# Kernel optimization log

Measured on AMD Instinct MI355X. Metric: run time of the kernel, lower is better.

The kernel has to match this reference:

```python
import jax, jax.numpy as jnp
import numpy as np

HID = 2048
HEADS = 16
HEAD = HID // HEADS  # 128
INTER = 8192
EPS = 1e-5
THETA = 10000.0
B, S = 2, 2048


def _layernorm(x, scale, bias):
    mu = jnp.mean(x, axis=-1, keepdims=True)
    var = jnp.var(x, axis=-1, keepdims=True)
    return (x - mu) * jax.lax.rsqrt(var + EPS) * scale + bias


def _rope(x, cos, sin):
    # x: [b,s,h,d]; adjacent pairs form complex numbers (per apply_rotary_emb)
    xr = x.reshape(*x.shape[:-1], HEAD // 2, 2)
    x0, x1 = xr[..., 0], xr[..., 1]
    o0 = x0 * cos - x1 * sin
    o1 = x0 * sin + x1 * cos
    return jnp.stack((o0, o1), axis=-1).reshape(x.shape)


def setup_inputs() -> dict:
    key = jax.random.key(0)
    ks = jax.random.split(key, 6)
    sc = 0.02
    return {
        "hidden_states": jax.random.normal(ks[0], (B, S, HID), jnp.float32),
        "attention_mask": jnp.zeros((B, 1, 1, S), jnp.float32),
        "w_qkv": (jax.random.normal(ks[1], (HID, 3 * HID), jnp.float32) * sc),
        "b_qkv": jnp.zeros((3 * HID,), jnp.float32),
        "w_o": (jax.random.normal(ks[2], (HID, HID), jnp.float32) * sc),
        "b_o": jnp.zeros((HID,), jnp.float32),
        "ln1_scale": jnp.ones((HID,), jnp.float32),
        "ln1_bias": jnp.zeros((HID,), jnp.float32),
        "ln2_scale": jnp.ones((HID,), jnp.float32),
        "ln2_bias": jnp.zeros((HID,), jnp.float32),
        "w_in": (jax.random.normal(ks[3], (HID, INTER), jnp.float32) * sc),
        "b_in": jnp.zeros((INTER,), jnp.float32),
        "w_out": (jax.random.normal(ks[4], (INTER, HID), jnp.float32) * sc),
        "b_out": jnp.zeros((HID,), jnp.float32),
    }


def reference(hidden_states, attention_mask, w_qkv, b_qkv, w_o, b_o,
              ln1_scale, ln1_bias, ln2_scale, ln2_bias,
              w_in, b_in, w_out, b_out):
    b, s, d = hidden_states.shape
    # ---- attention branch ----
    x1 = _layernorm(hidden_states, ln1_scale, ln1_bias)
    qkv = x1 @ w_qkv + b_qkv
    q, k, v = jnp.split(qkv, 3, axis=-1)
    q = q.reshape(b, s, HEADS, HEAD)
    k = k.reshape(b, s, HEADS, HEAD)
    v = v.reshape(b, s, HEADS, HEAD)
    # rotary embedding (complex pairing of adjacent elements)
    inv_freq = 1.0 / (THETA ** (jnp.arange(0, HEAD, 2, dtype=jnp.float32) / HEAD))
    freqs = jnp.arange(s, dtype=jnp.float32)[:, None] * inv_freq[None, :]  # [s, HEAD/2]
    cos = jnp.cos(freqs)[None, :, None, :]
    sin = jnp.sin(freqs)[None, :, None, :]
    q = _rope(q, cos, sin)
    k = _rope(k, cos, sin)
    # NOTE: source multiplies by sqrt(head_size) (faithful to original code)
    factor = jnp.sqrt(jnp.float32(HEAD))
    attn = jnp.einsum('bqhd,bkhd->bhqk', q, k) * factor  # [b,h,s,s]
    causal = jnp.tril(jnp.ones((s, s), dtype=bool))
    bias = jnp.where(causal, 0.0, jnp.finfo(jnp.float32).min)
    attn = attn + bias[None, None, :, :] + attention_mask
    p = jax.nn.softmax(attn, axis=-1)
    ao = jnp.einsum('bhqk,bkhd->bqhd', p, v).reshape(b, s, d)
    attn_out = ao @ w_o + b_o
    # ---- mlp branch (parallel residual) ----
    x2 = _layernorm(hidden_states, ln2_scale, ln2_bias)
    mlp = jax.nn.gelu(x2 @ w_in + b_in, approximate=False) @ w_out + b_out
    return mlp + hidden_states + attn_out
```

## Files before the change

kernel.cpp:

```cpp
#include <hip/hip_runtime.h>
#include <math.h>

#define HID 2048
#define NH 16
#define HD 128
#define INTER 8192
#define BB 2
#define SS 2048
#define MT (BB*SS)

typedef __bf16 bf16x8 __attribute__((ext_vector_type(8)));
typedef float f32x4 __attribute__((ext_vector_type(4)));
typedef unsigned short u16x8 __attribute__((ext_vector_type(8)));

__device__ __forceinline__ float bf2f(unsigned short u) {
  unsigned v = ((unsigned)u) << 16;
  return __builtin_bit_cast(float, v);
}
__device__ __forceinline__ unsigned short f2bf(float x) {
  unsigned u = __builtin_bit_cast(unsigned, x);
  u += 0x7fffu + ((u >> 16) & 1u);
  return (unsigned short)(u >> 16);
}
__device__ __forceinline__ void gll16(const void* g, const void* lds) {
  __builtin_amdgcn_global_load_lds(
      (const __attribute__((address_space(1))) void*)g,
      (__attribute__((address_space(3))) void*)lds, 16, 0, 0);
}

__global__ __launch_bounds__(256) void ln2k(
    const float* __restrict__ X, const float* __restrict__ s1,
    const float* __restrict__ b1, const float* __restrict__ s2,
    const float* __restrict__ b2, unsigned short* __restrict__ X1h,
    unsigned short* __restrict__ X1l, unsigned short* __restrict__ X2) {
  const int row = blockIdx.x;
  const int tid = threadIdx.x;
  const float* x = X + (long)row * HID;
  float4 v0 = ((const float4*)x)[tid * 2];
  float4 v1 = ((const float4*)x)[tid * 2 + 1];
  float s = v0.x + v0.y + v0.z + v0.w + v1.x + v1.y + v1.z + v1.w;
  float q = v0.x * v0.x + v0.y * v0.y + v0.z * v0.z + v0.w * v0.w +
            v1.x * v1.x + v1.y * v1.y + v1.z * v1.z + v1.w * v1.w;
#pragma unroll
  for (int off = 1; off < 64; off <<= 1) {
    s += __shfl_xor(s, off);
    q += __shfl_xor(q, off);
  }
  __shared__ float rs[4], rq[4];
  const int wid = tid >> 6, lane = tid & 63;
  if (lane == 0) { rs[wid] = s; rq[wid] = q; }
  __syncthreads();
  s = rs[0] + rs[1] + rs[2] + rs[3];
  q = rq[0] + rq[1] + rq[2] + rq[3];
  const float mu = s * (1.f / HID);
  const float var = q * (1.f / HID) - mu * mu;
  const float rstd = rsqrtf(var + 1e-5f);
  float xv[8] = {v0.x, v0.y, v0.z, v0.w, v1.x, v1.y, v1.z, v1.w};
  u16x8 o1h, o1l, o2;
#pragma unroll
  for (int e = 0; e < 8; e++) {
    const int j = tid * 8 + e;
    const float xn = (xv[e] - mu) * rstd;
    const float x1v = xn * s1[j] + b1[j];
    const unsigned short h = f2bf(x1v);
    o1h[e] = h;
    o1l[e] = f2bf(x1v - bf2f(h));
    o2[e] = f2bf(xn * s2[j] + b2[j]);
  }
  *(u16x8*)(X1h + (long)row * HID + tid * 8) = o1h;
  *(u16x8*)(X1l + (long)row * HID + tid * 8) = o1l;
  *(u16x8*)(X2 + (long)row * HID + tid * 8) = o2;
}

__global__ __launch_bounds__(256) void wtrans(const float* __restrict__ W,
                                              unsigned short* __restrict__ WT,
                                              int K, int N, int ldn, int coff) {
  (void)N;
  __shared__ float t[32][33];
  const int n0 = blockIdx.x * 32, k0 = blockIdx.y * 32;
  const int tx = threadIdx.x, ty = threadIdx.y;
#pragma unroll
  for (int r = 0; r < 4; r++)
    t[ty + r * 8][tx] = W[(long)(k0 + ty + r * 8) * ldn + coff + n0 + tx];
  __syncthreads();
#pragma unroll
  for (int r = 0; r < 4; r++)
    WT[(long)(n0 + ty + r * 8) * K + k0 + tx] = f2bf(t[tx][ty + r * 8]);
}

__global__ __launch_bounds__(256) void wtrans_hl(
    const float* __restrict__ W, unsigned short* __restrict__ WTh,
    unsigned short* __restrict__ WTl, int K, int ldn) {
  __shared__ float t[32][33];
  const int n0 = blockIdx.x * 32, k0 = blockIdx.y * 32;
  const int tx = threadIdx.x, ty = threadIdx.y;
#pragma unroll
  for (int r = 0; r < 4; r++)
    t[ty + r * 8][tx] = W[(long)(k0 + ty + r * 8) * ldn + n0 + tx];
  __syncthreads();
#pragma unroll
  for (int r = 0; r < 4; r++) {
    const float v = t[tx][ty + r * 8];
    const unsigned short h = f2bf(v);
    const long o = (long)(n0 + ty + r * 8) * K + k0 + tx;
    WTh[o] = h;
    WTl[o] = f2bf(v - bf2f(h));
  }
}

__global__ void rope_tab(float2* __restrict__ rope) {
  const int s = blockIdx.x, i = threadIdx.x;
  const double ang = (double)s * pow(10000.0, -(double)i / 64.0);
  rope[s * 64 + i] = make_float2((float)cos(ang), (float)sin(ang));
}

__global__ __launch_bounds__(256) void gemmqk(
    const unsigned short* __restrict__ Ah_, const unsigned short* __restrict__ Al_,
    const unsigned short* __restrict__ Bh_, const unsigned short* __restrict__ Bl_,
    const float* __restrict__ bias, const float2* __restrict__ rope,
    unsigned short* __restrict__ QH, unsigned short* __restrict__ QL,
    unsigned short* __restrict__ KH, unsigned short* __restrict__ KL) {
  __shared__ unsigned short Ash[128 * 64], Asl[128 * 64];
  __shared__ unsigned short Bsh[128 * 64], Bsl[128 * 64];
  const int K = HID;
  const int tid = threadIdx.x;
  const int wid = tid >> 6, lane = tid & 63;
  const int l16 = lane & 15, lhi = lane >> 4;
  const int bn = blockIdx.x, bm = blockIdx.y;
  const int wr = wid >> 1, wc = wid & 1;
  const long rA0 = (long)bm * 128;
  const long rB0 = (long)bn * 128;

  f32x4 acc[4][4] = {};

  for (int kt = 0; kt < K; kt += 64) {
#pragma unroll
    for (int i = 0; i < 4; i++) {
      const int lin = i * 4096 + wid * 1024 + (lane << 4);
      const int row = lin >> 7;
      const int cs = ((lin >> 4) & 7) ^ (row & 7);
      const int dst = i * 4096 + wid * 1024;
      const long ga = (rA0 + row) * (long)K + kt + cs * 8;
      const long gb = (rB0 + row) * (long)K + kt + cs * 8;
      gll16(Ah_ + ga, (const char*)Ash + dst);
      gll16(Al_ + ga, (const char*)Asl + dst);
      gll16(Bh_ + gb, (const char*)Bsh + dst);
      gll16(Bl_ + gb, (const char*)Bsl + dst);
    }
    __syncthreads();
#pragma unroll
    for (int ks = 0; ks < 2; ks++) {
      bf16x8 avh[4], avl[4], bvh[4], bvl[4];
#pragma unroll
      for (int m = 0; m < 4; m++) {
        const int row = wr * 64 + m * 16 + l16;
        const int ch = (ks * 4 + lhi) ^ (row & 7);
        avh[m] = *(const bf16x8*)((const char*)Ash + row * 128 + ch * 16);
        avl[m] = *(const bf16x8*)((const char*)Asl + row * 128 + ch * 16);
      }
#pragma unroll
      for (int n = 0; n < 4; n++) {
        const int row = wc * 64 + n * 16 + l16;
        const int ch = (ks * 4 + lhi) ^ (row & 7);
        bvh[n] = *(const bf16x8*)((const char*)Bsh + row * 128 + ch * 16);
        bvl[n] = *(const bf16x8*)((const char*)Bsl + row * 128 + ch * 16);
      }
#pragma unroll
      for (int m = 0; m < 4; m++)
#pragma unroll
        for (int n = 0; n < 4; n++) {
          acc[m][n] = __builtin_amdgcn_mfma_f32_16x16x32_bf16(avh[m], bvl[n],
                                                              acc[m][n], 0, 0, 0);
          acc[m][n] = __builtin_amdgcn_mfma_f32_16x16x32_bf16(avl[m], bvh[n],
                                                              acc[m][n], 0, 0, 0);
          acc[m][n] = __builtin_amdgcn_mfma_f32_16x16x32_bf16(avh[m], bvh[n],
                                                              acc[m][n], 0, 0, 0);
        }
    }
    __syncthreads();
  }

  const int b_ = (int)(rA0 >> 11);
#pragma unroll
  for (int m = 0; m < 4; m++) {
#pragma unroll
    for (int n = 0; n < 4; n++) {
      const int col = (int)rB0 + wc * 64 + n * 16 + l16;
      const float bsv = bias[col];
      const int i = (col & 127) >> 1;
      const int hh = (col >> 7) & 15;
      const int d = col & 127;
#pragma unroll
      for (int r = 0; r < 4; r++) {
        const int row = (int)rA0 + wr * 64 + m * 16 + lhi * 4 + r;
        const int srow = row & 2047;
        const float v = acc[m][n][r] + bsv;
        const float p = __shfl_xor(v, 1);
        const float2 cs = rope[srow * 64 + i];
        const float o = ((lane & 1) == 0) ? (v * cs.x - p * cs.y)
                                          : (p * cs.y + v * cs.x);
        const unsigned short hi = f2bf(o);
        const unsigned short lo = f2bf(o - bf2f(hi));
        const long dst = ((long)(b_ * NH + hh) * SS + srow) * HD + d;
        if (col < 2048) { QH[dst] = hi; QL[dst] = lo; }
        else            { KH[dst] = hi; KL[dst] = lo; }
      }
    }
  }
}

__global__ __launch_bounds__(256) void vtrans(
    const unsigned short* __restrict__ Vb, unsigned short* __restrict__ VTb) {
  __shared__ unsigned short t[32][33];
  const int bh = blockIdx.z, b = bh >> 4, h = bh & 15;
  const int d0 = blockIdx.x * 32, s0 = blockIdx.y * 32;
  const int tx = threadIdx.x, ty = threadIdx.y;
#pragma unroll
  for (int r = 0; r < 4; r++) {
    const int s = s0 + ty + r * 8;
    t[ty + r * 8][tx] = Vb[((long)(b * SS + s)) * HID + h * HD + d0 + tx];
  }
  __syncthreads();
#pragma unroll
  for (int r = 0; r < 4; r++) {
    const int d = d0 + ty + r * 8;
    VTb[((long)bh * HD + d) * SS + s0 + tx] = t[tx][ty + r * 8];
  }
}

template <int MODE>
__global__ __launch_bounds__(256) void gemm128(
    const unsigned short* __restrict__ A, const unsigned short* __restrict__ Bt,
    const float* __restrict__ bias, void* __restrict__ Cout, int M, int N,
    int K, const float* __restrict__ residF,
    const unsigned short* __restrict__ residB) {
  (void)M;
  __shared__ unsigned short As[128 * 64];
  __shared__ unsigned short Bs[128 * 64];
  const int tid = threadIdx.x;
  const int wid = tid >> 6, lane = tid & 63;
  const int l16 = lane & 15, lhi = lane >> 4;
  const int bn = blockIdx.x, bm = blockIdx.y;
  const int wr = wid >> 1, wc = wid & 1;
  const long rA0 = (long)bm * 128;
  const long rB0 = (long)bn * 128;

  f32x4 acc[4][4] = {};

  for (int kt = 0; kt < K; kt += 64) {
#pragma unroll
    for (int i = 0; i < 4; i++) {
      const int lin = i * 4096 + wid * 1024 + (lane << 4);
      const int row = lin >> 7;
      const int cs = ((lin >> 4) & 7) ^ (row & 7);
      gll16(A + (rA0 + row) * (long)K + kt + cs * 8,
            (const char*)As + (i * 4096 + wid * 1024));
      gll16(Bt + (rB0 + row) * (long)K + kt + cs * 8,
            (const char*)Bs + (i * 4096 + wid * 1024));
    }
    __syncthreads();
#pragma unroll
    for (int ks = 0; ks < 2; ks++) {
      bf16x8 av[4], bv[4];
#pragma unroll
      for (int m = 0; m < 4; m++) {
        const int row = wr * 64 + m * 16 + l16;
        const int ch = (ks * 4 + lhi) ^ (row & 7);
        av[m] = *(const bf16x8*)((const char*)As + row * 128 + ch * 16);
      }
#pragma unroll
      for (int n = 0; n < 4; n++) {
        const int row = wc * 64 + n * 16 + l16;
        const int ch = (ks * 4 + lhi) ^ (row & 7);
        bv[n] = *(const bf16x8*)((const char*)Bs + row * 128 + ch * 16);
      }
#pragma unroll
      for (int m = 0; m < 4; m++)
#pragma unroll
        for (int n = 0; n < 4; n++)
          acc[m][n] = __builtin_amdgcn_mfma_f32_16x16x32_bf16(av[m], bv[n],
                                                              acc[m][n], 0, 0, 0);
    }
    __syncthreads();
  }

#pragma unroll
  for (int m = 0; m < 4; m++) {
#pragma unroll
    for (int n = 0; n < 4; n++) {
      const long col = rB0 + wc * 64 + n * 16 + l16;
      const float bsv = bias[col];
#pragma unroll
      for (int r = 0; r < 4; r++) {
        const long row = rA0 + wr * 64 + m * 16 + lhi * 4 + r;
        float v = acc[m][n][r] + bsv;
        if (MODE == 1) v = 0.5f * v * (1.f + erff(v * 0.7071067811865475f));
        if (MODE == 2) {
          v += residF[row * N + col] + bf2f(residB[row * N + col]);
          ((float*)Cout)[row * N + col] = v;
        } else {
          ((unsigned short*)Cout)[row * N + col] = f2bf(v);
        }
      }
    }
  }
}

__global__ __launch_bounds__(256, 2) void flash(
    const unsigned short* __restrict__ QH, const unsigned short* __restrict__ QL,
    const unsigned short* __restrict__ KH, const unsigned short* __restrict__ KL,
    const unsigned short* __restrict__ VT, const float* __restrict__ amask,
    unsigned short* __restrict__ AO) {
  __shared__ unsigned short Kth[2][32 * 128];
  __shared__ unsigned short Ktl[2][32 * 128];
  __shared__ unsigned short Vt[2][128 * 32];
  __shared__ unsigned short Pl[4 * 1024];
  __shared__ float maskL[SS];
  const int bh = blockIdx.y;
  const int qt = (bh >= 16) ? blockIdx.x : (15 - blockIdx.x);
  const int b = bh >> 4, h = bh & 15;
  const int tid = threadIdx.x, wid = tid >> 6, lane = tid & 63;
  const int l16 = lane & 15, lhi = lane >> 4;
  const unsigned short* Qhb = QH + (long)bh * SS * HD;
  const unsigned short* Qlb = QL + (long)bh * SS * HD;
  const unsigned short* Khb = KH + (long)bh * SS * HD;
  const unsigned short* Klb = KL + (long)bh * SS * HD;
  const unsigned short* Vb = VT + (long)bh * HD * SS;
  const int q0 = qt * 128 + wid * 32;
  const float LOG2E = 1.4426950408889634f;
  const float SCL2 = 16.322232154552f;

  {
    const float4* mg = (const float4*)(amask + (long)b * SS);
    float4 m0 = mg[tid * 2], m1 = mg[tid * 2 + 1];
    m0.x *= LOG2E; m0.y *= LOG2E; m0.z *= LOG2E; m0.w *= LOG2E;
    m1.x *= LOG2E; m1.y *= LOG2E; m1.z *= LOG2E; m1.w *= LOG2E;
    ((float4*)maskL)[tid * 2] = m0;
    ((float4*)maskL)[tid * 2 + 1] = m1;
  }

  bf16x8 qfh[2][4], qfl[2][4];
#pragma unroll
  for (int mf = 0; mf < 2; mf++)
#pragma unroll
    for (int ks = 0; ks < 4; ks++) {
      const long o = (long)(q0 + mf * 16 + l16) * HD + ks * 32 + lhi * 8;
      qfh[mf][ks] = *(const bf16x8*)(Qhb + o);
      qfl[mf][ks] = *(const bf16x8*)(Qlb + o);
    }

  auto stage = [&](int kt2, int bu) {
#pragma unroll
    for (int i = 0; i < 2; i++) {
      const int lin = i * 4096 + wid * 1024 + (lane << 4);
      const int dst = i * 4096 + wid * 1024;
      {
        const int row = lin >> 8;
        const int cs = ((lin >> 4) & 15) ^ (row & 7);
        const long g = (long)(kt2 * 32 + row) * HD + cs * 8;
        gll16(Khb + g, (const char*)Kth[bu] + dst);
        gll16(Klb + g, (const char*)Ktl[bu] + dst);
      }
      {
        const int row = lin >> 6;
        const int cs = ((lin >> 4) & 3) ^ ((row >> 1) & 3);
        gll16(Vb + (long)row * SS + kt2 * 32 + cs * 8, (const char*)Vt[bu] + dst);
      }
    }
  };

  f32x4 accO[2][8] = {};
  float mrow[2][4], lrow[2][4];
#pragma unroll
  for (int mf = 0; mf < 2; mf++)
#pragma unroll
    for (int r = 0; r < 4; r++) { mrow[mf][r] = -3e38f; lrow[mf][r] = 0.f; }

  const int nkt = 4 * qt + 4;
  stage(0, 0);
  asm volatile("s_waitcnt lgkmcnt(0)" ::: "memory");
  int buf = 0;
  for (int kt = 0; kt < nkt; kt++) {
    if (kt + 1 < nkt) {
      stage(kt + 1, buf ^ 1);
      asm volatile("s_waitcnt vmcnt(6)" ::: "memory");
    } else {
      asm volatile("s_waitcnt vmcnt(0)" ::: "memory");
    }
    __builtin_amdgcn_s_barrier();

    f32x4 accS[2][2] = {};
    __builtin_amdgcn_s_setprio(1);
#pragma unroll
    for (int ks = 0; ks < 4; ks++) {
      bf16x8 bkh[2], bkl[2];
#pragma unroll
      for (int nf = 0; nf < 2; nf++) {
        const int row = nf * 16 + l16;
        const int ch = (ks * 4 + lhi) ^ (row & 7);
        bkh[nf] = *(const bf16x8*)((const char*)Kth[buf] + row * 256 + ch * 16);
        bkl[nf] = *(const bf16x8*)((const char*)Ktl[buf] + row * 256 + ch * 16);
      }
#pragma unroll
      for (int mf = 0; mf < 2; mf++)
#pragma unroll
        for (int nf = 0; nf < 2; nf++) {
          accS[mf][nf] = __builtin_amdgcn_mfma_f32_16x16x32_bf16(
              qfh[mf][ks], bkl[nf], accS[mf][nf], 0, 0, 0);
          accS[mf][nf] = __builtin_amdgcn_mfma_f32_16x16x32_bf16(
              qfl[mf][ks], bkh[nf], accS[mf][nf], 0, 0, 0);
          accS[mf][nf] = __builtin_amdgcn_mfma_f32_16x16x32_bf16(
              qfh[mf][ks], bkh[nf], accS[mf][nf], 0, 0, 0);
        }
    }
    __builtin_amdgcn_s_setprio(0);

    float mk[2];
    mk[0] = maskL[kt * 32 + l16];
    mk[1] = maskL[kt * 32 + 16 + l16];
#pragma unroll
    for (int mf = 0; mf < 2; mf++)
#pragma unroll
      for (int nf = 0; nf < 2; nf++)
#pragma unroll
        for (int r = 0; r < 4; r++) {
          const int key = kt * 32 + nf * 16 + l16;
          const int qg = q0 + mf * 16 + lhi * 4 + r;
          const float sv = accS[mf][nf][r] * SCL2 + mk[nf];
          accS[mf][nf][r] = (key > qg) ? -1e30f : sv;
        }

    float mx[2][4];
#pragma unroll
    for (int mf = 0; mf < 2; mf++)
#pragma unroll
      for (int r = 0; r < 4; r++) {
        float m0 = fmaxf(accS[mf][0][r], accS[mf][1][r]);
        m0 = fmaxf(m0, __shfl_xor(m0, 1));
        m0 = fmaxf(m0, __shfl_xor(m0, 2));
        m0 = fmaxf(m0, __shfl_xor(m0, 4));
        m0 = fmaxf(m0, __shfl_xor(m0, 8));
        mx[mf][r] = m0;
      }
    bool defer = true;
#pragma unroll
    for (int mf = 0; mf < 2; mf++)
#pragma unroll
      for (int r = 0; r < 4; r++)
        defer = defer && (mx[mf][r] <= mrow[mf][r] + 8.f);
    if (!__all(defer)) {
#pragma unroll
      for (int mf = 0; mf < 2; mf++)
#pragma unroll
        for (int r = 0; r < 4; r++) {
          const float mnew = fmaxf(mrow[mf][r], mx[mf][r]);
          const float alpha = exp2f(mrow[mf][r] - mnew);
          mrow[mf][r] = mnew;
          lrow[mf][r] *= alpha;
#pragma unroll
          for (int nf2 = 0; nf2 < 8; nf2++) accO[mf][nf2][r] *= alpha;
        }
    }
#pragma unroll
    for (int mf = 0; mf < 2; mf++)
#pragma unroll
      for (int r = 0; r < 4; r++) {
        const int rowl = mf * 16 + lhi * 4 + r;
        const int qg = q0 + rowl;
        float rsum = 0.f;
#pragma unroll
        for (int nf = 0; nf < 2; nf++) {
          const int key = kt * 32 + nf * 16 + l16;
          const float p =
              (key > qg) ? 0.f : exp2f(accS[mf][nf][r] - mrow[mf][r]);
          rsum += p;
          const int colv = nf * 16 + l16;
          const int slot = (colv >> 3) ^ ((rowl >> 1) & 3);
          *(unsigned short*)((char*)Pl + wid * 2048 + rowl * 64 + slot * 16 +
                             (colv & 7) * 2) = f2bf(p);
        }
        rsum += __shfl_xor(rsum, 1);
        rsum += __shfl_xor(rsum, 2);
        rsum += __shfl_xor(rsum, 4);
        rsum += __shfl_xor(rsum, 8);
        lrow[mf][r] += rsum;
      }

    __builtin_amdgcn_s_setprio(1);
    {
      bf16x8 pa[2];
#pragma unroll
      for (int mf = 0; mf < 2; mf++) {
        const int rowp = mf * 16 + l16;
        const int ch = lhi ^ ((rowp >> 1) & 3);
        pa[mf] = *(const bf16x8*)((const char*)Pl + wid * 2048 + rowp * 64 +
                                  ch * 16);
      }
#pragma unroll
      for (int nf2 = 0; nf2 < 8; nf2++) {
        const int rowv = nf2 * 16 + l16;
        const int ch = lhi ^ ((rowv >> 1) & 3);
        bf16x8 vv =
            *(const bf16x8*)((const char*)Vt[buf] + rowv * 64 + ch * 16);
#pragma unroll
        for (int mf = 0; mf < 2; mf++)
          accO[mf][nf2] = __builtin_amdgcn_mfma_f32_16x16x32_bf16(
              pa[mf], vv, accO[mf][nf2], 0, 0, 0);
      }
    }
    __builtin_amdgcn_s_setprio(0);
    __builtin_amdgcn_s_barrier();
    buf ^= 1;
  }

#pragma unroll
  for (int mf = 0; mf < 2; mf++)
#pragma unroll
    for (int nf2 = 0; nf2 < 8; nf2++)
#pragma unroll
      for (int r = 0; r < 4; r++) {
        const int qg = q0 + mf * 16 + lhi * 4 + r;
        const int d = nf2 * 16 + l16;
        const float v = accO[mf][nf2][r] / lrow[mf][r];
        AO[((long)(b * SS + qg)) * HID + h * HD + d] = f2bf(v);
      }
}

extern "C" void kernel_launch(void* const* d_in, const int* in_sizes, int n_in,
                              void* d_out, int out_size, void* d_ws,
                              size_t ws_size, hipStream_t stream) {
  (void)in_sizes; (void)n_in; (void)out_size;
  const float* hidden = (const float*)d_in[0];
  const float* amask = (const float*)d_in[1];
  const float* w_qkv = (const float*)d_in[2];
  const float* b_qkv = (const float*)d_in[3];
  const float* w_o = (const float*)d_in[4];
  const float* b_o = (const float*)d_in[5];
  const float* ln1s = (const float*)d_in[6];
  const float* ln1b = (const float*)d_in[7];
  const float* ln2s = (const float*)d_in[8];
  const float* ln2b = (const float*)d_in[9];
  const float* w_in = (const float*)d_in[10];
  const float* b_in = (const float*)d_in[11];
  const float* w_out = (const float*)d_in[12];
  const float* b_out = (const float*)d_in[13];

  char* ws = (char*)d_ws;
  unsigned short* X1h = (unsigned short*)(ws + 0);
  unsigned short* X1l = (unsigned short*)(ws + 16777216);
  unsigned short* X2  = (unsigned short*)(ws + 33554432);
  unsigned short* W1h = (unsigned short*)(ws + 50331648);
  unsigned short* W1l = (unsigned short*)(ws + 67108864);
  unsigned short* WE  = (unsigned short*)(ws + 83886080);
  unsigned short* QHb = (unsigned short*)(ws + 92274688);
  unsigned short* QLb = (unsigned short*)(ws + 109051904);
  unsigned short* KHb = (unsigned short*)(ws + 125829120);
  unsigned short* KLb = (unsigned short*)(ws + 142606336);
  unsigned short* VTb = (unsigned short*)(ws + 159383552);
  unsigned short* ATT = (unsigned short*)(ws + 176160768);
  float2* ROPE = (float2*)(ws + 192937984);
  if (ws_size < 193986560) return;

  unsigned short* Vbf = X1l;
  unsigned short* AO = X1h;
  unsigned short* WD = W1h;
  unsigned short* H1 = QHb;

  ln2k<<<MT, 256, 0, stream>>>(hidden, ln1s, ln1b, ln2s, ln2b, X1h, X1l, X2);
  rope_tab<<<SS, 64, 0, stream>>>(ROPE);
  wtrans_hl<<<dim3(128, 64), dim3(32, 8), 0, stream>>>(w_qkv, W1h, W1l,
                                                       HID, 3 * HID);
  gemmqk<<<dim3(32, 32), 256, 0, stream>>>(X1h, X1l, W1h, W1l, b_qkv, ROPE,
                                           QHb, QLb, KHb, KLb);
  wtrans<<<dim3(64, 64), dim3(32, 8), 0, stream>>>(w_qkv, WE, HID, HID,
                                                   3 * HID, 2 * HID);
  gemm128<0><<<dim3(16, 32), 256, 0, stream>>>(X1h, WE, b_qkv + 2 * HID, Vbf,
                                               MT, HID, HID, nullptr, nullptr);
  vtrans<<<dim3(4, 64, 32), dim3(32, 8), 0, stream>>>(Vbf, VTb);
  flash<<<dim3(16, 32), 256, 0, stream>>>(QHb, QLb, KHb, KLb, VTb, amask, AO);
  wtrans<<<dim3(64, 64), dim3(32, 8), 0, stream>>>(w_o, WE, HID, HID, HID, 0);
  gemm128<0><<<dim3(16, 32), 256, 0, stream>>>(AO, WE, b_o, ATT, MT, HID, HID,
                                               nullptr, nullptr);
  wtrans<<<dim3(256, 64), dim3(32, 8), 0, stream>>>(w_in, WD, HID, INTER,
                                                    INTER, 0);
  gemm128<1><<<dim3(64, 32), 256, 0, stream>>>(X2, WD, b_in, H1, MT, INTER,
                                               HID, nullptr, nullptr);
  wtrans<<<dim3(64, 256), dim3(32, 8), 0, stream>>>(w_out, WD, INTER, HID,
                                                    HID, 0);
  gemm128<2><<<dim3(16, 32), 256, 0, stream>>>(H1, WD, b_out, d_out, MT, HID,
                                               INTER, hidden, ATT);
}
```

Before: 935.7 us.

## Replace split-bf16 QK path with fp16 and fuse V into one QKV GEMM

Swaps the three-MFMA hi/lo bf16 emulation for the Q/K projection and QK^T scores for single fp16 MFMAs. This removes the lo-part buffers, their loads and two-thirds of those MFMAs. V is now computed inside the same fused QKV GEMM instead of a separate GEMM and weight transpose. The flash kernel also skips score and PV work for fully masked causal tiles and raises its occupancy hint to 3. The cost is fp16 precision, with its range and overflow risk, where hi/lo bf16 used to be.

```diff
diff --git a/kernel.cpp b/kernel.cpp
--- a/kernel.cpp
+++ b/kernel.cpp
@@ -10,6 +10,7 @@
 #define MT (BB*SS)
 
 typedef __bf16 bf16x8 __attribute__((ext_vector_type(8)));
+typedef _Float16 f16x8 __attribute__((ext_vector_type(8)));
 typedef float f32x4 __attribute__((ext_vector_type(4)));
 typedef unsigned short u16x8 __attribute__((ext_vector_type(8)));
 
@@ -22,6 +23,10 @@
   u += 0x7fffu + ((u >> 16) & 1u);
   return (unsigned short)(u >> 16);
 }
+__device__ __forceinline__ unsigned short f2h(float x) {
+  _Float16 h = (_Float16)x;
+  return __builtin_bit_cast(unsigned short, h);
+}
 __device__ __forceinline__ void gll16(const void* g, const void* lds) {
   __builtin_amdgcn_global_load_lds(
       (const __attribute__((address_space(1))) void*)g,
@@ -31,8 +36,8 @@
 __global__ __launch_bounds__(256) void ln2k(
     const float* __restrict__ X, const float* __restrict__ s1,
     const float* __restrict__ b1, const float* __restrict__ s2,
-    const float* __restrict__ b2, unsigned short* __restrict__ X1h,
-    unsigned short* __restrict__ X1l, unsigned short* __restrict__ X2) {
+    const float* __restrict__ b2, unsigned short* __restrict__ X1f,
+    unsigned short* __restrict__ X2) {
   const int row = blockIdx.x;
   const int tid = threadIdx.x;
   const float* x = X + (long)row * HID;
@@ -56,22 +61,19 @@
   const float var = q * (1.f / HID) - mu * mu;
   const float rstd = rsqrtf(var + 1e-5f);
   float xv[8] = {v0.x, v0.y, v0.z, v0.w, v1.x, v1.y, v1.z, v1.w};
-  u16x8 o1h, o1l, o2;
+  u16x8 o1, o2;
 #pragma unroll
   for (int e = 0; e < 8; e++) {
     const int j = tid * 8 + e;
     const float xn = (xv[e] - mu) * rstd;
-    const float x1v = xn * s1[j] + b1[j];
-    const unsigned short h = f2bf(x1v);
-    o1h[e] = h;
-    o1l[e] = f2bf(x1v - bf2f(h));
+    o1[e] = f2h(xn * s1[j] + b1[j]);
     o2[e] = f2bf(xn * s2[j] + b2[j]);
   }
-  *(u16x8*)(X1h + (long)row * HID + tid * 8) = o1h;
-  *(u16x8*)(X1l + (long)row * HID + tid * 8) = o1l;
+  *(u16x8*)(X1f + (long)row * HID + tid * 8) = o1;
   *(u16x8*)(X2 + (long)row * HID + tid * 8) = o2;
 }
 
+template <bool F16>
 __global__ __launch_bounds__(256) void wtrans(const float* __restrict__ W,
                                               unsigned short* __restrict__ WT,
                                               int K, int N, int ldn, int coff) {
@@ -84,27 +86,9 @@
     t[ty + r * 8][tx] = W[(long)(k0 + ty + r * 8) * ldn + coff + n0 + tx];
   __syncthreads();
 #pragma unroll
-  for (int r = 0; r < 4; r++)
-    WT[(long)(n0 + ty + r * 8) * K + k0 + tx] = f2bf(t[tx][ty + r * 8]);
-}
-
-__global__ __launch_bounds__(256) void wtrans_hl(
-    const float* __restrict__ W, unsigned short* __restrict__ WTh,
-    unsigned short* __restrict__ WTl, int K, int ldn) {
-  __shared__ float t[32][33];
-  const int n0 = blockIdx.x * 32, k0 = blockIdx.y * 32;
-  const int tx = threadIdx.x, ty = threadIdx.y;
-#pragma unroll
-  for (int r = 0; r < 4; r++)
-    t[ty + r * 8][tx] = W[(long)(k0 + ty + r * 8) * ldn + n0 + tx];
-  __syncthreads();
-#pragma unroll
   for (int r = 0; r < 4; r++) {
     const float v = t[tx][ty + r * 8];
-    const unsigned short h = f2bf(v);
-    const long o = (long)(n0 + ty + r * 8) * K + k0 + tx;
-    WTh[o] = h;
-    WTl[o] = f2bf(v - bf2f(h));
+    WT[(long)(n0 + ty + r * 8) * K + k0 + tx] = F16 ? f2h(v) : f2bf(v);
   }
 }
 
@@ -114,14 +98,13 @@
   rope[s * 64 + i] = make_float2((float)cos(ang), (float)sin(ang));
 }
 
-__global__ __launch_bounds__(256) void gemmqk(
-    const unsigned short* __restrict__ Ah_, const unsigned short* __restrict__ Al_,
-    const unsigned short* __restrict__ Bh_, const unsigned short* __restrict__ Bl_,
+__global__ __launch_bounds__(256) void gemmqkv(
+    const unsigned short* __restrict__ A, const unsigned short* __restrict__ Bt,
     const float* __restrict__ bias, const float2* __restrict__ rope,
-    unsigned short* __restrict__ QH, unsigned short* __restrict__ QL,
-    unsigned short* __restrict__ KH, unsigned short* __restrict__ KL) {
-  __shared__ unsigned short Ash[128 * 64], Asl[128 * 64];
-  __shared__ unsigned short Bsh[128 * 64], Bsl[128 * 64];
+    unsigned short* __restrict__ QF, unsigned short* __restrict__ KF,
+    unsigned short* __restrict__ Vb) {
+  __shared__ unsigned short As[128 * 64];
+  __shared__ unsigned short Bs[128 * 64];
   const int K = HID;
   const int tid = threadIdx.x;
   const int wid = tid >> 6, lane = tid & 63;
@@ -139,43 +122,33 @@
       const int lin = i * 4096 + wid * 1024 + (lane << 4);
       const int row = lin >> 7;
       const int cs = ((lin >> 4) & 7) ^ (row & 7);
-      const int dst = i * 4096 + wid * 1024;
-      const long ga = (rA0 + row) * (long)K + kt + cs * 8;
-      const long gb = (rB0 + row) * (long)K + kt + cs * 8;
-      gll16(Ah_ + ga, (const char*)Ash + dst);
-      gll16(Al_ + ga, (const char*)Asl + dst);
-      gll16(Bh_ + gb, (const char*)Bsh + dst);
-      gll16(Bl_ + gb, (const char*)Bsl + dst);
+      gll16(A + (rA0 + row) * (long)K + kt + cs * 8,
+            (const char*)As + (i * 4096 + wid * 1024));
+      gll16(Bt + (rB0 + row) * (long)K + kt + cs * 8,
+            (const char*)Bs + (i * 4096 + wid * 1024));
     }
     __syncthreads();
 #pragma unroll
     for (int ks = 0; ks < 2; ks++) {
-      bf16x8 avh[4], avl[4], bvh[4], bvl[4];
+      f16x8 av[4], bv[4];
 #pragma unroll
       for (int m = 0; m < 4; m++) {
         const int row = wr * 64 + m * 16 + l16;
         const int ch = (ks * 4 + lhi) ^ (row & 7);
-        avh[m] = *(const bf16x8*)((const char*)Ash + row * 128 + ch * 16);
-        avl[m] = *(const bf16x8*)((const char*)Asl + row * 128 + ch * 16);
+        av[m] = *(const f16x8*)((const char*)As + row * 128 + ch * 16);
       }
 #pragma unroll
       for (int n = 0; n < 4; n++) {
         const int row = wc * 64 + n * 16 + l16;
         const int ch = (ks * 4 + lhi) ^ (row & 7);
-        bvh[n] = *(const bf16x8*)((const char*)Bsh + row * 128 + ch * 16);
-        bvl[n] = *(const bf16x8*)((const char*)Bsl + row * 128 + ch * 16);
+        bv[n] = *(const f16x8*)((const char*)Bs + row * 128 + ch * 16);
       }
 #pragma unroll
       for (int m = 0; m < 4; m++)
 #pragma unroll
-        for (int n = 0; n < 4; n++) {
-          acc[m][n] = __builtin_amdgcn_mfma_f32_16x16x32_bf16(avh[m], bvl[n],
-                                                              acc[m][n], 0, 0, 0);
-          acc[m][n] = __builtin_amdgcn_mfma_f32_16x16x32_bf16(avl[m], bvh[n],
-                                                              acc[m][n], 0, 0, 0);
-          acc[m][n] = __builtin_amdgcn_mfma_f32_16x16x32_bf16(avh[m], bvh[n],
-                                                              acc[m][n], 0, 0, 0);
-        }
+        for (int n = 0; n < 4; n++)
+          acc[m][n] = __builtin_amdgcn_mfma_f32_16x16x32_f16(av[m], bv[n],
+                                                             acc[m][n], 0, 0, 0);
     }
     __syncthreads();
   }
@@ -187,23 +160,25 @@
     for (int n = 0; n < 4; n++) {
       const int col = (int)rB0 + wc * 64 + n * 16 + l16;
       const float bsv = bias[col];
-      const int i = (col & 127) >> 1;
-      const int hh = (col >> 7) & 15;
-      const int d = col & 127;
+      const int cq = col & 2047;
+      const int i = (cq & 127) >> 1;
+      const int hh = (cq >> 7) & 15;
+      const int d = cq & 127;
 #pragma unroll
       for (int r = 0; r < 4; r++) {
         const int row = (int)rA0 + wr * 64 + m * 16 + lhi * 4 + r;
         const int srow = row & 2047;
         const float v = acc[m][n][r] + bsv;
-        const float p = __shfl_xor(v, 1);
-        const float2 cs = rope[srow * 64 + i];
-        const float o = ((lane & 1) == 0) ? (v * cs.x - p * cs.y)
-                                          : (p * cs.y + v * cs.x);
-        const unsigned short hi = f2bf(o);
-        const unsigned short lo = f2bf(o - bf2f(hi));
-        const long dst = ((long)(b_ * NH + hh) * SS + srow) * HD + d;
-        if (col < 2048) { QH[dst] = hi; QL[dst] = lo; }
-        else            { KH[dst] = hi; KL[dst] = lo; }
+        if (col < 4096) {
+          const float p = __shfl_xor(v, 1);
+          const float2 cs = rope[srow * 64 + i];
+          const float o = ((lane & 1) == 0) ? (v * cs.x - p * cs.y)
+                                            : (p * cs.y + v * cs.x);
+          unsigned short* dst = (col < 2048) ? QF : KF;
+          dst[((long)(b_ * NH + hh) * SS + srow) * HD + d] = f2h(o);
+        } else {
+          Vb[(long)row * HID + (col - 4096)] = f2bf(v);
+        }
       }
     }
   }
@@ -306,13 +281,11 @@
   }
 }
 
-__global__ __launch_bounds__(256, 2) void flash(
-    const unsigned short* __restrict__ QH, const unsigned short* __restrict__ QL,
-    const unsigned short* __restrict__ KH, const unsigned short* __restrict__ KL,
+__global__ __launch_bounds__(256, 3) void flash(
+    const unsigned short* __restrict__ QF, const unsigned short* __restrict__ KF,
     const unsigned short* __restrict__ VT, const float* __restrict__ amask,
     unsigned short* __restrict__ AO) {
-  __shared__ unsigned short Kth[2][32 * 128];
-  __shared__ unsigned short Ktl[2][32 * 128];
+  __shared__ unsigned short Kt[2][32 * 128];
   __shared__ unsigned short Vt[2][128 * 32];
   __shared__ unsigned short Pl[4 * 1024];
   __shared__ float maskL[SS];
@@ -321,10 +294,8 @@
   const int b = bh >> 4, h = bh & 15;
   const int tid = threadIdx.x, wid = tid >> 6, lane = tid & 63;
   const int l16 = lane & 15, lhi = lane >> 4;
-  const unsigned short* Qhb = QH + (long)bh * SS * HD;
-  const unsigned short* Qlb = QL + (long)bh * SS * HD;
-  const unsigned short* Khb = KH + (long)bh * SS * HD;
-  const unsigned short* Klb = KL + (long)bh * SS * HD;
+  const unsigned short* Qfb = QF + (long)bh * SS * HD;
+  const unsigned short* Kfb = KF + (long)bh * SS * HD;
   const unsigned short* Vb = VT + (long)bh * HD * SS;
   const int q0 = qt * 128 + wid * 32;
   const float LOG2E = 1.4426950408889634f;
@@ -339,15 +310,13 @@
     ((float4*)maskL)[tid * 2 + 1] = m1;
   }
 
-  bf16x8 qfh[2][4], qfl[2][4];
+  f16x8 qf[2][4];
 #pragma unroll
   for (int mf = 0; mf < 2; mf++)
 #pragma unroll
-    for (int ks = 0; ks < 4; ks++) {
-      const long o = (long)(q0 + mf * 16 + l16) * HD + ks * 32 + lhi * 8;
-      qfh[mf][ks] = *(const bf16x8*)(Qhb + o);
-      qfl[mf][ks] = *(const bf16x8*)(Qlb + o);
-    }
+    for (int ks = 0; ks < 4; ks++)
+      qf[mf][ks] = *(const f16x8*)(Qfb + (long)(q0 + mf * 16 + l16) * HD +
+                                   ks * 32 + lhi * 8);
 
   auto stage = [&](int kt2, int bu) {
 #pragma unroll
@@ -357,9 +326,8 @@
       {
         const int row = lin >> 8;
         const int cs = ((lin >> 4) & 15) ^ (row & 7);
-        const long g = (long)(kt2 * 32 + row) * HD + cs * 8;
-        gll16(Khb + g, (const char*)Kth[bu] + dst);
-        gll16(Klb + g, (const char*)Ktl[bu] + dst);
+        gll16(Kfb + (long)(kt2 * 32 + row) * HD + cs * 8,
+              (const char*)Kt[bu] + dst);
       }
       {
         const int row = lin >> 6;
@@ -383,132 +351,129 @@
   for (int kt = 0; kt < nkt; kt++) {
     if (kt + 1 < nkt) {
       stage(kt + 1, buf ^ 1);
-      asm volatile("s_waitcnt vmcnt(6)" ::: "memory");
+      asm volatile("s_waitcnt vmcnt(4)" ::: "memory");
     } else {
       asm volatile("s_waitcnt vmcnt(0)" ::: "memory");
     }
     __builtin_amdgcn_s_barrier();
 
-    f32x4 accS[2][2] = {};
-    __builtin_amdgcn_s_setprio(1);
-#pragma unroll
-    for (int ks = 0; ks < 4; ks++) {
-      bf16x8 bkh[2], bkl[2];
-#pragma unroll
-      for (int nf = 0; nf < 2; nf++) {
-        const int row = nf * 16 + l16;
-        const int ch = (ks * 4 + lhi) ^ (row & 7);
-        bkh[nf] = *(const bf16x8*)((const char*)Kth[buf] + row * 256 + ch * 16);
-        bkl[nf] = *(const bf16x8*)((const char*)Ktl[buf] + row * 256 + ch * 16);
-      }
+    const bool active = (kt * 32 <= q0 + 31);
+    if (active) {
+      f32x4 accS[2][2] = {};
+      __builtin_amdgcn_s_setprio(1);
+#pragma unroll
+      for (int ks = 0; ks < 4; ks++) {
+        f16x8 bk[2];
+#pragma unroll
+        for (int nf = 0; nf < 2; nf++) {
+          const int row = nf * 16 + l16;
+          const int ch = (ks * 4 + lhi) ^ (row & 7);
+          bk[nf] = *(const f16x8*)((const char*)Kt[buf] + row * 256 + ch * 16);
+        }
+#pragma unroll
+        for (int mf = 0; mf < 2; mf++)
+#pragma unroll
+          for (int nf = 0; nf < 2; nf++)
+            accS[mf][nf] = __builtin_amdgcn_mfma_f32_16x16x32_f16(
+                qf[mf][ks], bk[nf], accS[mf][nf], 0, 0, 0);
+      }
+      __builtin_amdgcn_s_setprio(0);
+
+      float mk[2];
+      mk[0] = maskL[kt * 32 + l16];
+      mk[1] = maskL[kt * 32 + 16 + l16];
 #pragma unroll
       for (int mf = 0; mf < 2; mf++)
 #pragma unroll
-        for (int nf = 0; nf < 2; nf++) {
-          accS[mf][nf] = __builtin_amdgcn_mfma_f32_16x16x32_bf16(
-              qfh[mf][ks], bkl[nf], accS[mf][nf], 0, 0, 0);
-          accS[mf][nf] = __builtin_amdgcn_mfma_f32_16x16x32_bf16(
-              qfl[mf][ks], bkh[nf], accS[mf][nf], 0, 0, 0);
-          accS[mf][nf] = __builtin_amdgcn_mfma_f32_16x16x32_bf16(
-              qfh[mf][ks], bkh[nf], accS[mf][nf], 0, 0, 0);
-        }
-    }
-    __builtin_amdgcn_s_setprio(0);
-
-    float mk[2];
-    mk[0] = maskL[kt * 32 + l16];
-    mk[1] = maskL[kt * 32 + 16 + l16];
-#pragma unroll
-    for (int mf = 0; mf < 2; mf++)
-#pragma unroll
-      for (int nf = 0; nf < 2; nf++)
+        for (int nf = 0; nf < 2; nf++)
+#pragma unroll
+          for (int r = 0; r < 4; r++) {
+            const int key = kt * 32 + nf * 16 + l16;
+            const int qg = q0 + mf * 16 + lhi * 4 + r;
+            const float sv = accS[mf][nf][r] * SCL2 + mk[nf];
+            accS[mf][nf][r] = (key > qg) ? -1e30f : sv;
+          }
+
+      float mx[2][4];
+#pragma unroll
+      for (int mf = 0; mf < 2; mf++)
 #pragma unroll
         for (int r = 0; r < 4; r++) {
-          const int key = kt * 32 + nf * 16 + l16;
-          const int qg = q0 + mf * 16 + lhi * 4 + r;
-          const float sv = accS[mf][nf][r] * SCL2 + mk[nf];
-          accS[mf][nf][r] = (key > qg) ? -1e30f : sv;
-        }
-
-    float mx[2][4];
-#pragma unroll
-    for (int mf = 0; mf < 2; mf++)
-#pragma unroll
-      for (int r = 0; r < 4; r++) {
-        float m0 = fmaxf(accS[mf][0][r], accS[mf][1][r]);
-        m0 = fmaxf(m0, __shfl_xor(m0, 1));
-        m0 = fmaxf(m0, __shfl_xor(m0, 2));
-        m0 = fmaxf(m0, __shfl_xor(m0, 4));
-        m0 = fmaxf(m0, __shfl_xor(m0, 8));
-        mx[mf][r] = m0;
-      }
-    bool defer = true;
-#pragma unroll
-    for (int mf = 0; mf < 2; mf++)
-#pragma unroll
-      for (int r = 0; r < 4; r++)
-        defer = defer && (mx[mf][r] <= mrow[mf][r] + 8.f);
-    if (!__all(defer)) {
+          float m0 = fmaxf(accS[mf][0][r], accS[mf][1][r]);
+          m0 = fmaxf(m0, __shfl_xor(m0, 1));
+          m0 = fmaxf(m0, __shfl_xor(m0, 2));
+          m0 = fmaxf(m0, __shfl_xor(m0, 4));
+          m0 = fmaxf(m0, __shfl_xor(m0, 8));
+          mx[mf][r] = m0;
+        }
+      bool defer = true;
 #pragma unroll
       for (int mf = 0; mf < 2; mf++)
 #pragma unroll
+        for (int r = 0; r < 4; r++)
+          defer = defer && (mx[mf][r] <= mrow[mf][r] + 8.f);
+      if (!__all(defer)) {
+#pragma unroll
+        for (int mf = 0; mf < 2; mf++)
+#pragma unroll
+          for (int r = 0; r < 4; r++) {
+            const float mnew = fmaxf(mrow[mf][r], mx[mf][r]);
+            const float alpha = exp2f(mrow[mf][r] - mnew);
+            mrow[mf][r] = mnew;
+            lrow[mf][r] *= alpha;
+#pragma unroll
+            for (int nf2 = 0; nf2 < 8; nf2++) accO[mf][nf2][r] *= alpha;
+          }
+      }
+#pragma unroll
+      for (int mf = 0; mf < 2; mf++)
+#pragma unroll
         for (int r = 0; r < 4; r++) {
-          const float mnew = fmaxf(mrow[mf][r], mx[mf][r]);
-          const float alpha = exp2f(mrow[mf][r] - mnew);
-          mrow[mf][r] = mnew;
-          lrow[mf][r] *= alpha;
-#pragma unroll
-          for (int nf2 = 0; nf2 < 8; nf2++) accO[mf][nf2][r] *= alpha;
-        }
-    }
-#pragma unroll
-    for (int mf = 0; mf < 2; mf++)
-#pragma unroll
-      for (int r = 0; r < 4; r++) {
-        const int rowl = mf * 16 + lhi * 4 + r;
-        const int qg = q0 + rowl;
-        float rsum = 0.f;
-#pragma unroll
-        for (int nf = 0; nf < 2; nf++) {
-          const int key = kt * 32 + nf * 16 + l16;
-          const float p =
-              (key > qg) ? 0.f : exp2f(accS[mf][nf][r] - mrow[mf][r]);
-          rsum += p;
-          const int colv = nf * 16 + l16;
-          const int slot = (colv >> 3) ^ ((rowl >> 1) & 3);
-          *(unsigned short*)((char*)Pl + wid * 2048 + rowl * 64 + slot * 16 +
-                             (colv & 7) * 2) = f2bf(p);
-        }
-        rsum += __shfl_xor(rsum, 1);
-        rsum += __shfl_xor(rsum, 2);
-        rsum += __shfl_xor(rsum, 4);
-        rsum += __shfl_xor(rsum, 8);
-        lrow[mf][r] += rsum;
-      }
-
-    __builtin_amdgcn_s_setprio(1);
-    {
-      bf16x8 pa[2];
-#pragma unroll
-      for (int mf = 0; mf < 2; mf++) {
-        const int rowp = mf * 16 + l16;
-        const int ch = lhi ^ ((rowp >> 1) & 3);
-        pa[mf] = *(const bf16x8*)((const char*)Pl + wid * 2048 + rowp * 64 +
-                                  ch * 16);
-      }
-#pragma unroll
-      for (int nf2 = 0; nf2 < 8; nf2++) {
-        const int rowv = nf2 * 16 + l16;
-        const int ch = lhi ^ ((rowv >> 1) & 3);
-        bf16x8 vv =
-            *(const bf16x8*)((const char*)Vt[buf] + rowv * 64 + ch * 16);
-#pragma unroll
-        for (int mf = 0; mf < 2; mf++)
-          accO[mf][nf2] = __builtin_amdgcn_mfma_f32_16x16x32_bf16(
-              pa[mf], vv, accO[mf][nf2], 0, 0, 0);
-      }
-    }
-    __builtin_amdgcn_s_setprio(0);
+          const int rowl = mf * 16 + lhi * 4 + r;
+          const int qg = q0 + rowl;
+          float rsum = 0.f;
+#pragma unroll
+          for (int nf = 0; nf < 2; nf++) {
+            const int key = kt * 32 + nf * 16 + l16;
+            const float p =
+                (key > qg) ? 0.f : exp2f(accS[mf][nf][r] - mrow[mf][r]);
+            rsum += p;
+            const int colv = nf * 16 + l16;
+            const int slot = (colv >> 3) ^ ((rowl >> 1) & 3);
+            *(unsigned short*)((char*)Pl + wid * 2048 + rowl * 64 + slot * 16 +
+                               (colv & 7) * 2) = f2bf(p);
+          }
+          rsum += __shfl_xor(rsum, 1);
+          rsum += __shfl_xor(rsum, 2);
+          rsum += __shfl_xor(rsum, 4);
+          rsum += __shfl_xor(rsum, 8);
+          lrow[mf][r] += rsum;
+        }
+
+      __builtin_amdgcn_s_setprio(1);
+      {
+        bf16x8 pa[2];
+#pragma unroll
+        for (int mf = 0; mf < 2; mf++) {
+          const int rowp = mf * 16 + l16;
+          const int ch = lhi ^ ((rowp >> 1) & 3);
+          pa[mf] = *(const bf16x8*)((const char*)Pl + wid * 2048 + rowp * 64 +
+                                    ch * 16);
+        }
+#pragma unroll
+        for (int nf2 = 0; nf2 < 8; nf2++) {
+          const int rowv = nf2 * 16 + l16;
+          const int ch = lhi ^ ((rowv >> 1) & 3);
+          bf16x8 vv =
+              *(const bf16x8*)((const char*)Vt[buf] + rowv * 64 + ch * 16);
+#pragma unroll
+          for (int mf = 0; mf < 2; mf++)
+            accO[mf][nf2] = __builtin_amdgcn_mfma_f32_16x16x32_bf16(
+                pa[mf], vv, accO[mf][nf2], 0, 0, 0);
+        }
+      }
+      __builtin_amdgcn_s_setprio(0);
+    }
     __builtin_amdgcn_s_barrier();
     buf ^= 1;
   }
@@ -546,47 +511,39 @@
   const float* b_out = (const float*)d_in[13];
 
   char* ws = (char*)d_ws;
-  unsigned short* X1h = (unsigned short*)(ws + 0);
-  unsigned short* X1l = (unsigned short*)(ws + 16777216);
-  unsigned short* X2  = (unsigned short*)(ws + 33554432);
-  unsigned short* W1h = (unsigned short*)(ws + 50331648);
-  unsigned short* W1l = (unsigned short*)(ws + 67108864);
-  unsigned short* WE  = (unsigned short*)(ws + 83886080);
-  unsigned short* QHb = (unsigned short*)(ws + 92274688);
-  unsigned short* QLb = (unsigned short*)(ws + 109051904);
-  unsigned short* KHb = (unsigned short*)(ws + 125829120);
-  unsigned short* KLb = (unsigned short*)(ws + 142606336);
-  unsigned short* VTb = (unsigned short*)(ws + 159383552);
-  unsigned short* ATT = (unsigned short*)(ws + 176160768);
-  float2* ROPE = (float2*)(ws + 192937984);
-  if (ws_size < 193986560) return;
-
-  unsigned short* Vbf = X1l;
-  unsigned short* AO = X1h;
-  unsigned short* WD = W1h;
-  unsigned short* H1 = QHb;
-
-  ln2k<<<MT, 256, 0, stream>>>(hidden, ln1s, ln1b, ln2s, ln2b, X1h, X1l, X2);
+  unsigned short* X1f = (unsigned short*)(ws + 0);
+  unsigned short* X2  = (unsigned short*)(ws + 16777216);
+  unsigned short* Vbf = (unsigned short*)(ws + 33554432);
+  unsigned short* WQ  = (unsigned short*)(ws + 50331648);
+  unsigned short* QFb = (unsigned short*)(ws + 75497472);
+  unsigned short* KFb = (unsigned short*)(ws + 92274688);
+  unsigned short* VTb = (unsigned short*)(ws + 109051904);
+  unsigned short* ATT = (unsigned short*)(ws + 125829120);
+  unsigned short* WD  = (unsigned short*)(ws + 142606336);
+  float2* ROPE = (float2*)(ws + 176160768);
+  if (ws_size < 177209344) return;
+
+  unsigned short* AO = X1f;
+  unsigned short* H1 = WQ;
+
+  ln2k<<<MT, 256, 0, stream>>>(hidden, ln1s, ln1b, ln2s, ln2b, X1f, X2);
   rope_tab<<<SS, 64, 0, stream>>>(ROPE);
-  wtrans_hl<<<dim3(128, 64), dim3(32, 8), 0, stream>>>(w_qkv, W1h, W1l,
-                                                       HID, 3 * HID);
-  gemmqk<<<dim3(32, 32), 256, 0, stream>>>(X1h, X1l, W1h, W1l, b_qkv, ROPE,
-                                           QHb, QLb, KHb, KLb);
-  wtrans<<<dim3(64, 64), dim3(32, 8), 0, stream>>>(w_qkv, WE, HID, HID,
-                                                   3 * HID, 2 * HID);
-  gemm128<0><<<dim3(16, 32), 256, 0, stream>>>(X1h, WE, b_qkv + 2 * HID, Vbf,
-                                               MT, HID, HID, nullptr, nullptr);
+  wtrans<true><<<dim3(192, 64), dim3(32, 8), 0, stream>>>(w_qkv, WQ, HID,
+                                                          3 * HID, 3 * HID, 0);
+  gemmqkv<<<dim3(48, 32), 256, 0, stream>>>(X1f, WQ, b_qkv, ROPE, QFb, KFb,
+                                            Vbf);
   vtrans<<<dim3(4, 64, 32), dim3(32, 8), 0, stream>>>(Vbf, VTb);
-  flash<<<dim3(16, 32), 256, 0, stream>>>(QHb, QLb, KHb, KLb, VTb, amask, AO);
-  wtrans<<<dim3(64, 64), dim3(32, 8), 0, stream>>>(w_o, WE, HID, HID, HID, 0);
-  gemm128<0><<<dim3(16, 32), 256, 0, stream>>>(AO, WE, b_o, ATT, MT, HID, HID,
+  flash<<<dim3(16, 32), 256, 0, stream>>>(QFb, KFb, VTb, amask, AO);
+  wtrans<false><<<dim3(64, 64), dim3(32, 8), 0, stream>>>(w_o, WD, HID, HID,
+                                                          HID, 0);
+  gemm128<0><<<dim3(16, 32), 256, 0, stream>>>(AO, WD, b_o, ATT, MT, HID, HID,
                                                nullptr, nullptr);
-  wtrans<<<dim3(256, 64), dim3(32, 8), 0, stream>>>(w_in, WD, HID, INTER,
-                                                    INTER, 0);
+  wtrans<false><<<dim3(256, 64), dim3(32, 8), 0, stream>>>(w_in, WD, HID,
+                                                           INTER, INTER, 0);
   gemm128<1><<<dim3(64, 32), 256, 0, stream>>>(X2, WD, b_in, H1, MT, INTER,
                                                HID, nullptr, nullptr);
-  wtrans<<<dim3(64, 256), dim3(32, 8), 0, stream>>>(w_out, WD, INTER, HID,
-                                                    HID, 0);
+  wtrans<false><<<dim3(64, 256), dim3(32, 8), 0, stream>>>(w_out, WD, INTER,
+                                                           HID, HID, 0);
   gemm128<2><<<dim3(16, 32), 256, 0, stream>>>(H1, WD, b_out, d_out, MT, HID,
                                                INTER, hidden, ATT);
 }
```

Result: slower. 993.5 us (+6.2%).
